# Optimization experiments

Measured on AMD Instinct MI355X. Metric: run time of the kernel, lower is better.

## Reference

```python
import jax, jax.numpy as jnp
import numpy as np

N_NODES = 100000
N_EDGES = 1600000
D_IN = 32
D_OUT = 64


def setup_inputs() -> dict:
    key = jax.random.key(0)
    ks = jax.random.split(key, 6)
    x = jax.random.normal(ks[0], (N_NODES, D_IN), dtype=jnp.float32)
    edge_row = jax.random.randint(ks[1], (N_EDGES,), 0, N_NODES, dtype=jnp.int32)
    edge_col = jax.random.randint(ks[2], (N_EDGES,), 0, N_NODES, dtype=jnp.int32)
    edge_val = jax.random.uniform(ks[3], (N_EDGES,), dtype=jnp.float32)
    W = jax.random.normal(ks[4], (D_IN, D_OUT), dtype=jnp.float32) * (1.0 / np.sqrt(D_IN))
    b = jax.random.normal(ks[5], (D_OUT,), dtype=jnp.float32) * 0.01
    return {"x": x, "edge_row": edge_row, "edge_col": edge_col,
            "edge_val": edge_val, "W": W, "b": b, "k": 4}


def _spmm(edge_row, edge_col, edge_val, x, n_nodes):
    # out[i] = sum_{e: row[e]==i} val[e] * x[col[e]]  (sparse adj @ x)
    gathered = edge_val[:, None] * x[edge_col]  # [E, D]
    return jax.ops.segment_sum(gathered, edge_row, num_segments=n_nodes)


def reference(x, edge_row, edge_col, edge_val, W, b, k):
    # k-hop propagation: x <- A @ x, repeated k times (k is a static Python int)
    for _ in range(k):
        x = _spmm(edge_row, edge_col, edge_val, x, N_NODES)
    # final dense linear: x @ W + b
    return x @ W + b
```

## Files before the change

kernel.cpp:

```cpp
#include <hip/hip_runtime.h>
#include <hip/hip_fp16.h>

#define N_NODES 100000
#define N_EDGES 1600000
#define D_IN 32
#define D_OUT 64

#define RPB 200
#define NBKT 500
#define CAP 4096
#define EPT 16
#define SCT 256
#define EPB (EPT * SCT)
#define SBLOCKS ((N_EDGES + EPB - 1) / EPB)
#define N2 (N_NODES * D_IN / 2)
#define CVT_BLOCKS ((N2 + 255) / 256)

#define COL_BITS 17
#define COL_MASK ((1u << COL_BITS) - 1u)
#define VAL_SCALE 32767.0f
#define VAL_INV (1.0f / 32767.0f)

typedef unsigned int uv2 __attribute__((ext_vector_type(2)));
typedef unsigned int uv4 __attribute__((ext_vector_type(4)));

__global__ void init_bcur(int* __restrict__ bcur) {
    int i = threadIdx.x;
    if (i < NBKT) bcur[i] = i * CAP;
}

__global__ void scatter_chunks(const int* __restrict__ erow,
                               const int* __restrict__ ecol,
                               const float* __restrict__ eval_,
                               int* __restrict__ bcur,
                               int2* __restrict__ staged,
                               const float2* __restrict__ xf,
                               unsigned int* __restrict__ xh) {
    if (blockIdx.x >= SBLOCKS) {
        int i = (blockIdx.x - SBLOCKS) * blockDim.x + threadIdx.x;
        if (i < N2) {
            float2 f = xf[i];
            __half2 h = __floats2half2_rn(f.x, f.y);
            xh[i] = *(unsigned int*)&h;
        }
        return;
    }
    __shared__ int h[NBKT];
    __shared__ int cb[NBKT];
    for (int i = threadIdx.x; i < NBKT; i += blockDim.x) h[i] = 0;
    __syncthreads();
    int base = blockIdx.x * EPB;
    unsigned pk[EPT]; float val[EPT]; int brk[EPT];
#pragma unroll
    for (int k = 0; k < EPT; ++k) {
        int e = base + k * SCT + threadIdx.x;
        if (e < N_EDGES) {
            int r = __builtin_nontemporal_load(&erow[e]);
            int c = __builtin_nontemporal_load(&ecol[e]);
            float v = __builtin_nontemporal_load(&eval_[e]);
            int b = r / RPB;
            int rl = r - b * RPB;
            int rank = atomicAdd(&h[b], 1);
            pk[k] = ((unsigned)rl << COL_BITS) | (unsigned)c;
            val[k] = v;
            brk[k] = b | (rank << 9);
        } else brk[k] = -1;
    }
    __syncthreads();
    for (int i = threadIdx.x; i < NBKT; i += blockDim.x) {
        int c = h[i];
        if (c) cb[i] = atomicAdd(&bcur[i], c);
    }
    __syncthreads();
#pragma unroll
    for (int k = 0; k < EPT; ++k) {
        if (brk[k] >= 0) {
            int b = brk[k] & 511;
            int rank = brk[k] >> 9;
            int2 p; p.x = (int)pk[k]; p.y = __float_as_int(val[k]);
            staged[cb[b] + rank] = p;
        }
    }
}

__global__ void sort_bucket(const int* __restrict__ bcur,
                            const int2* __restrict__ staged,
                            unsigned int* __restrict__ epack,
                            int2* __restrict__ row_rng) {
    __shared__ int hist[RPB];
    __shared__ int offs[RPB];
    __shared__ int cur[RPB];
    __shared__ int ptot;
    int b = blockIdx.x;
    int s0 = b * CAP, s1 = bcur[b];
    for (int i = threadIdx.x; i < RPB; i += blockDim.x) hist[i] = 0;
    __syncthreads();
    for (int e = s0 + threadIdx.x; e < s1; e += blockDim.x) {
        unsigned w = (unsigned)staged[e].x;
        atomicAdd(&hist[w >> COL_BITS], 1);
    }
    __syncthreads();
    if (threadIdx.x == 0) {
        int run = 0;
        for (int i = 0; i < RPB; ++i) {
            offs[i] = run;
            run += (hist[i] + 7) & ~7;
        }
        ptot = run;
    }
    __syncthreads();
    int r0 = b * RPB;
    int pt = ptot;
    for (int i = threadIdx.x; i < pt; i += blockDim.x) epack[s0 + i] = 0u;
    for (int i = threadIdx.x; i < RPB; i += blockDim.x) {
        int st = s0 + offs[i];
        int2 rr; rr.x = st; rr.y = st + ((hist[i] + 7) & ~7);
        row_rng[r0 + i] = rr;
        cur[i] = offs[i];
    }
    __syncthreads();
    for (int e = s0 + threadIdx.x; e < s1; e += blockDim.x) {
        int2 p = staged[e];
        unsigned w = (unsigned)p.x;
        int rl = (int)(w >> COL_BITS);
        int pos = atomicAdd(&cur[rl], 1);
        float v = __int_as_float(p.y);
        unsigned q = (unsigned)(int)(v * VAL_SCALE + 0.5f);
        epack[s0 + pos] = (q << COL_BITS) | (w & COL_MASK);
    }
}

__global__ void spmm_csr(const int2* __restrict__ row_rng,
                         const uv4* __restrict__ epack4,
                         const uv2* __restrict__ xin,
                         uv2* __restrict__ xout) {
    int lane = threadIdx.x & 63;
    int wave = threadIdx.x >> 6;
    int qt = lane >> 4;
    int g  = (lane >> 3) & 1;
    int j  = lane & 7;
    int r = (blockIdx.x * (blockDim.x >> 6) + wave) * 4 + qt;
    if (r >= N_NODES) return;
    int2 pe = row_rng[r];
    int p0 = pe.x, p1 = pe.y;
    float4 a0 = {0.f,0.f,0.f,0.f}, a1 = {0.f,0.f,0.f,0.f};
    float4 a2 = {0.f,0.f,0.f,0.f}, a3 = {0.f,0.f,0.f,0.f};
    for (int eb = p0; eb < p1; eb += 8) {
        uv4 q = epack4[(eb >> 2) + g];
        unsigned q0 = q.x, q1 = q.y, q2 = q.z, q3 = q.w;
        uv2 w0 = xin[(q0 & COL_MASK) * 8 + j];
        uv2 w1 = xin[(q1 & COL_MASK) * 8 + j];
        uv2 w2 = xin[(q2 & COL_MASK) * 8 + j];
        uv2 w3 = xin[(q3 & COL_MASK) * 8 + j];
        float v0 = (float)(q0 >> COL_BITS) * VAL_INV;
        float v1 = (float)(q1 >> COL_BITS) * VAL_INV;
        float v2 = (float)(q2 >> COL_BITS) * VAL_INV;
        float v3 = (float)(q3 >> COL_BITS) * VAL_INV;
        unsigned w0x = w0.x, w0y = w0.y, w1x = w1.x, w1y = w1.y;
        unsigned w2x = w2.x, w2y = w2.y, w3x = w3.x, w3y = w3.y;
        float2 f0a = __half22float2(*(__half2*)&w0x), f0b = __half22float2(*(__half2*)&w0y);
        float2 f1a = __half22float2(*(__half2*)&w1x), f1b = __half22float2(*(__half2*)&w1y);
        float2 f2a = __half22float2(*(__half2*)&w2x), f2b = __half22float2(*(__half2*)&w2y);
        float2 f3a = __half22float2(*(__half2*)&w3x), f3b = __half22float2(*(__half2*)&w3y);
        a0.x += v0 * f0a.x; a0.y += v0 * f0a.y; a0.z += v0 * f0b.x; a0.w += v0 * f0b.y;
        a1.x += v1 * f1a.x; a1.y += v1 * f1a.y; a1.z += v1 * f1b.x; a1.w += v1 * f1b.y;
        a2.x += v2 * f2a.x; a2.y += v2 * f2a.y; a2.z += v2 * f2b.x; a2.w += v2 * f2b.y;
        a3.x += v3 * f3a.x; a3.y += v3 * f3a.y; a3.z += v3 * f3b.x; a3.w += v3 * f3b.y;
    }
    float4 acc;
    acc.x = (a0.x + a1.x) + (a2.x + a3.x);
    acc.y = (a0.y + a1.y) + (a2.y + a3.y);
    acc.z = (a0.z + a1.z) + (a2.z + a3.z);
    acc.w = (a0.w + a1.w) + (a2.w + a3.w);
    acc.x += __shfl_xor(acc.x, 8, 64);
    acc.y += __shfl_xor(acc.y, 8, 64);
    acc.z += __shfl_xor(acc.z, 8, 64);
    acc.w += __shfl_xor(acc.w, 8, 64);
    if (g == 0) {
        __half2 o0 = __floats2half2_rn(acc.x, acc.y);
        __half2 o1 = __floats2half2_rn(acc.z, acc.w);
        uv2 w;
        w.x = *(unsigned int*)&o0;
        w.y = *(unsigned int*)&o1;
        xout[r * 8 + j] = w;
    }
}

__global__ void linear_bias(const __half2* __restrict__ xin,
                            const float* __restrict__ W,
                            const float* __restrict__ b,
                            float* __restrict__ out) {
    __shared__ float sW[D_IN * D_OUT];
    __shared__ float sb[D_OUT];
    for (int i = threadIdx.x; i < D_IN * D_OUT; i += blockDim.x) sW[i] = W[i];
    if (threadIdx.x < D_OUT) sb[threadIdx.x] = b[threadIdx.x];
    __syncthreads();

    int r = blockIdx.x * 4 + (threadIdx.x >> 6);
    int j = threadIdx.x & 63;
    if (r >= N_NODES) return;

    const __half2* xr = xin + r * (D_IN / 2);
    float acc = sb[j];
#pragma unroll
    for (int d = 0; d < D_IN / 2; ++d) {
        float2 f = __half22float2(xr[d]);
        acc += f.x * sW[(2 * d) * D_OUT + j] + f.y * sW[(2 * d + 1) * D_OUT + j];
    }
    out[r * D_OUT + j] = acc;
}

extern "C" void kernel_launch(void* const* d_in, const int* in_sizes, int n_in,
                              void* d_out, int out_size, void* d_ws, size_t ws_size,
                              hipStream_t stream) {
    const float* x     = (const float*)d_in[0];
    const int*   erow  = (const int*)d_in[1];
    const int*   ecol  = (const int*)d_in[2];
    const float* eval_ = (const float*)d_in[3];
    const float* W     = (const float*)d_in[4];
    const float* b     = (const float*)d_in[5];
    float* out = (float*)d_out;

    unsigned int* xh0 = (unsigned int*)d_ws;
    unsigned int* xh1 = xh0 + (size_t)N2;
    int* bcur = (int*)(xh1 + (size_t)N2);
    int2* row_rng = (int2*)(bcur + 512);
    int2* staged = row_rng + N_NODES;
    unsigned int* epack = (unsigned int*)(staged + (size_t)NBKT * CAP);

    const int threads = 256;

    init_bcur<<<1, 512, 0, stream>>>(bcur);
    scatter_chunks<<<SBLOCKS + CVT_BLOCKS, SCT, 0, stream>>>(
        erow, ecol, eval_, bcur, staged, (const float2*)x, xh0);
    sort_bucket<<<NBKT, threads, 0, stream>>>(bcur, staged, epack, row_rng);

    const int rows_per_block = (threads / 64) * 4;
    const int sblocks = (N_NODES + rows_per_block - 1) / rows_per_block;
    const unsigned int* cur = xh0;
    for (int hop = 0; hop < 4; ++hop) {
        unsigned int* dst = (hop & 1) ? xh0 : xh1;
        spmm_csr<<<sblocks, threads, 0, stream>>>((const int2*)row_rng,
                                                  (const uv4*)epack,
                                                  (const uv2*)cur, (uv2*)dst);
        cur = dst;
    }

    const int lin_blocks = (N_NODES + 3) / 4;
    linear_bias<<<lin_blocks, 256, 0, stream>>>((const __half2*)cur, W, b, out);
}
```

Before: 243.4 us.

## Prefetch edge packs, pad only tails, and grid-stride the linear kernel

The edge-zeroing pass in sort_bucket is replaced: instead of clearing the whole padded range before placing edges, only the tail slots of each row are cleared after placement, which avoids double writes. The SpMM kernel gains a software prefetch of the next edge-pack vector, launch bounds, no row bound check, and per-hop template instantiations. The linear kernel reads 16-byte vectors and loops grid-stride over 2048 blocks. Bucket capacity is raised to leave room for padding overflow. The prefetch reads one vector past each row's end, which stays inside the workspace but costs an extra load.

```diff
diff --git a/kernel.cpp b/kernel.cpp
--- a/kernel.cpp
+++ b/kernel.cpp
@@ -8,13 +8,14 @@
 
 #define RPB 200
 #define NBKT 500
-#define CAP 4096
+#define CAP 4608
 #define EPT 16
 #define SCT 256
 #define EPB (EPT * SCT)
 #define SBLOCKS ((N_EDGES + EPB - 1) / EPB)
 #define N2 (N_NODES * D_IN / 2)
 #define CVT_BLOCKS ((N2 + 255) / 256)
+#define NGRP (N_NODES / 4)
 
 #define COL_BITS 17
 #define COL_MASK ((1u << COL_BITS) - 1u)
@@ -90,7 +91,6 @@
     __shared__ int hist[RPB];
     __shared__ int offs[RPB];
     __shared__ int cur[RPB];
-    __shared__ int ptot;
     int b = blockIdx.x;
     int s0 = b * CAP, s1 = bcur[b];
     for (int i = threadIdx.x; i < RPB; i += blockDim.x) hist[i] = 0;
@@ -106,12 +106,9 @@
             offs[i] = run;
             run += (hist[i] + 7) & ~7;
         }
-        ptot = run;
     }
     __syncthreads();
     int r0 = b * RPB;
-    int pt = ptot;
-    for (int i = threadIdx.x; i < pt; i += blockDim.x) epack[s0 + i] = 0u;
     for (int i = threadIdx.x; i < RPB; i += blockDim.x) {
         int st = s0 + offs[i];
         int2 rr; rr.x = st; rr.y = st + ((hist[i] + 7) & ~7);
@@ -128,25 +125,32 @@
         unsigned q = (unsigned)(int)(v * VAL_SCALE + 0.5f);
         epack[s0 + pos] = (q << COL_BITS) | (w & COL_MASK);
     }
-}
-
-__global__ void spmm_csr(const int2* __restrict__ row_rng,
-                         const uv4* __restrict__ epack4,
-                         const uv2* __restrict__ xin,
-                         uv2* __restrict__ xout) {
+    __syncthreads();
+    for (int i = threadIdx.x; i < RPB; i += blockDim.x) {
+        int end = offs[i] + ((hist[i] + 7) & ~7);
+        for (int k = cur[i]; k < end; ++k) epack[s0 + k] = 0u;
+    }
+}
+
+template <int HOP>
+__global__ void __launch_bounds__(256, 8)
+spmm_hop(const int2* __restrict__ row_rng,
+         const uv4* __restrict__ epack4,
+         const uv2* __restrict__ xin,
+         uv2* __restrict__ xout) {
     int lane = threadIdx.x & 63;
     int wave = threadIdx.x >> 6;
     int qt = lane >> 4;
     int g  = (lane >> 3) & 1;
     int j  = lane & 7;
-    int r = (blockIdx.x * (blockDim.x >> 6) + wave) * 4 + qt;
-    if (r >= N_NODES) return;
+    int r = (blockIdx.x * 4 + wave) * 4 + qt;
     int2 pe = row_rng[r];
     int p0 = pe.x, p1 = pe.y;
     float4 a0 = {0.f,0.f,0.f,0.f}, a1 = {0.f,0.f,0.f,0.f};
     float4 a2 = {0.f,0.f,0.f,0.f}, a3 = {0.f,0.f,0.f,0.f};
+    uv4 q = epack4[(p0 >> 2) + g];
     for (int eb = p0; eb < p1; eb += 8) {
-        uv4 q = epack4[(eb >> 2) + g];
+        uv4 qn = epack4[((eb + 8) >> 2) + g];
         unsigned q0 = q.x, q1 = q.y, q2 = q.z, q3 = q.w;
         uv2 w0 = xin[(q0 & COL_MASK) * 8 + j];
         uv2 w1 = xin[(q1 & COL_MASK) * 8 + j];
@@ -166,6 +170,7 @@
         a1.x += v1 * f1a.x; a1.y += v1 * f1a.y; a1.z += v1 * f1b.x; a1.w += v1 * f1b.y;
         a2.x += v2 * f2a.x; a2.y += v2 * f2a.y; a2.z += v2 * f2b.x; a2.w += v2 * f2b.y;
         a3.x += v3 * f3a.x; a3.y += v3 * f3a.y; a3.z += v3 * f3b.x; a3.w += v3 * f3b.y;
+        q = qn;
     }
     float4 acc;
     acc.x = (a0.x + a1.x) + (a2.x + a3.x);
@@ -186,7 +191,7 @@
     }
 }
 
-__global__ void linear_bias(const __half2* __restrict__ xin,
+__global__ void linear_bias(const uv4* __restrict__ xin,
                             const float* __restrict__ W,
                             const float* __restrict__ b,
                             float* __restrict__ out) {
@@ -196,18 +201,25 @@
     if (threadIdx.x < D_OUT) sb[threadIdx.x] = b[threadIdx.x];
     __syncthreads();
 
-    int r = blockIdx.x * 4 + (threadIdx.x >> 6);
+    int sub = threadIdx.x >> 6;
     int j = threadIdx.x & 63;
-    if (r >= N_NODES) return;
-
-    const __half2* xr = xin + r * (D_IN / 2);
-    float acc = sb[j];
-#pragma unroll
-    for (int d = 0; d < D_IN / 2; ++d) {
-        float2 f = __half22float2(xr[d]);
-        acc += f.x * sW[(2 * d) * D_OUT + j] + f.y * sW[(2 * d + 1) * D_OUT + j];
-    }
-    out[r * D_OUT + j] = acc;
+    for (int grp = blockIdx.x; grp < NGRP; grp += gridDim.x) {
+        int r = grp * 4 + sub;
+        const uv4* xr4 = xin + (size_t)r * 4;
+        float acc = sb[j];
+#pragma unroll
+        for (int qd = 0; qd < 4; ++qd) {
+            uv4 v = xr4[qd];
+            unsigned vw[4] = {v.x, v.y, v.z, v.w};
+#pragma unroll
+            for (int w = 0; w < 4; ++w) {
+                float2 f = __half22float2(*(__half2*)&vw[w]);
+                int d = 8 * qd + 2 * w;
+                acc += f.x * sW[d * D_OUT + j] + f.y * sW[(d + 1) * D_OUT + j];
+            }
+        }
+        out[r * D_OUT + j] = acc;
+    }
 }
 
 extern "C" void kernel_launch(void* const* d_in, const int* in_sizes, int n_in,
@@ -225,7 +237,7 @@
     unsigned int* xh1 = xh0 + (size_t)N2;
     int* bcur = (int*)(xh1 + (size_t)N2);
     int2* row_rng = (int2*)(bcur + 512);
-    int2* staged = row_rng + N_NODES;
+    int2* staged = (int2*)(row_rng + N_NODES);
     unsigned int* epack = (unsigned int*)(staged + (size_t)NBKT * CAP);
 
     const int threads = 256;
@@ -235,17 +247,15 @@
         erow, ecol, eval_, bcur, staged, (const float2*)x, xh0);
     sort_bucket<<<NBKT, threads, 0, stream>>>(bcur, staged, epack, row_rng);
 
-    const int rows_per_block = (threads / 64) * 4;
-    const int sblocks = (N_NODES + rows_per_block - 1) / rows_per_block;
-    const unsigned int* cur = xh0;
-    for (int hop = 0; hop < 4; ++hop) {
-        unsigned int* dst = (hop & 1) ? xh0 : xh1;
-        spmm_csr<<<sblocks, threads, 0, stream>>>((const int2*)row_rng,
-                                                  (const uv4*)epack,
-                                                  (const uv2*)cur, (uv2*)dst);
-        cur = dst;
-    }
-
-    const int lin_blocks = (N_NODES + 3) / 4;
-    linear_bias<<<lin_blocks, 256, 0, stream>>>((const __half2*)cur, W, b, out);
-}
+    const int sblocks = N_NODES / 16;
+    spmm_hop<0><<<sblocks, threads, 0, stream>>>(row_rng, (const uv4*)epack,
+                                                 (const uv2*)xh0, (uv2*)xh1);
+    spmm_hop<1><<<sblocks, threads, 0, stream>>>(row_rng, (const uv4*)epack,
+                                                 (const uv2*)xh1, (uv2*)xh0);
+    spmm_hop<2><<<sblocks, threads, 0, stream>>>(row_rng, (const uv4*)epack,
+                                                 (const uv2*)xh0, (uv2*)xh1);
+    spmm_hop<3><<<sblocks, threads, 0, stream>>>(row_rng, (const uv4*)epack,
+                                                 (const uv2*)xh1, (uv2*)xh0);
+
+    linear_bias<<<2048, 256, 0, stream>>>((const uv4*)xh0, W, b, out);
+}
```

Result: faster. 226.8 us (-6.8%).
